# Optimization experiments

Measured on AMD Instinct MI355X. Metric: run time of the kernel, lower is better.

The kernel has to match this reference:

```python
import jax, jax.numpy as jnp
import numpy as np

MAXLEN = 30
VOCAB_SIZE = 20000
THOUGHT = 1200
WORD = 620
BATCH = 130  # decoder uses B-2 = 128 sequences


def setup_inputs() -> dict:
    key = jax.random.key(0)
    ks = jax.random.split(key, 8)
    s_ih = 1.0 / np.sqrt(WORD)
    return {
        "thoughts": jax.random.normal(ks[0], (BATCH, THOUGHT), dtype=jnp.float32),
        "embed_table": jax.random.normal(ks[1], (VOCAB_SIZE, WORD), dtype=jnp.float32),
        "W_ih": jax.random.uniform(ks[2], (4 * WORD, 2 * THOUGHT + WORD), jnp.float32, -s_ih, s_ih),
        "W_hh": jax.random.uniform(ks[3], (4 * WORD, WORD), jnp.float32, -s_ih, s_ih),
        "b_ih": jax.random.uniform(ks[4], (4 * WORD,), jnp.float32, -s_ih, s_ih),
        "b_hh": jax.random.uniform(ks[5], (4 * WORD,), jnp.float32, -s_ih, s_ih),
        "Ww": jax.random.uniform(ks[6], (VOCAB_SIZE, WORD), jnp.float32, -s_ih, s_ih),
        "bw": jax.random.uniform(ks[7], (VOCAB_SIZE,), jnp.float32, -s_ih, s_ih),
    }


def reference(thoughts, embed_table, W_ih, W_hh, b_ih, b_hh, Ww, bw):
    # context: concat(thoughts_prev, thoughts_next) -> [B-2, 2*THOUGHT]
    ctx = jnp.concatenate([thoughts[:-2], thoughts[2:]], axis=1)
    n = ctx.shape[0]
    h0 = jnp.zeros((n, WORD), dtype=thoughts.dtype)  # (h,c) reset to 0 each step

    def step(last_word, _):
        x = jnp.concatenate([ctx, last_word], axis=1)  # [n, 3020]
        # LSTM cell with zero initial state (original discards state each step)
        gates = x @ W_ih.T + b_ih + h0 @ W_hh.T + b_hh  # [n, 4*WORD]
        i, f, g, o = jnp.split(gates, 4, axis=1)
        c = jax.nn.sigmoid(i) * jnp.tanh(g)  # f-gate irrelevant, c_prev = 0
        h = jax.nn.sigmoid(o) * jnp.tanh(c)  # [n, WORD]
        logits = h @ Ww.T + bw               # [n, VOCAB]
        idx = jnp.argmax(logits, axis=1)
        new_last = embed_table[idx]          # greedy-decoded word embedding
        return new_last, h

    _, hs = jax.lax.scan(step, h0, None, length=MAXLEN)  # [MAXLEN, n, WORD]
    pred = jnp.einsum("tnw,vw->tnv", hs, Ww) + bw        # [MAXLEN, n, VOCAB]
    return jnp.transpose(pred, (1, 0, 2))                 # [n, MAXLEN, VOCAB]
```

## Files before the change

### kernel.cpp

```cpp
#include <hip/hip_runtime.h>
#include <math.h>

#define VOCAB 20000
#define WORD 620
#define NSEQ 128
#define TMAX 30
#define CTXK 2400
#define XK 3020
#define NBLK 256

typedef unsigned long long u64;
typedef __attribute__((ext_vector_type(8))) short short8;
typedef __attribute__((ext_vector_type(4))) float f32x4;

__device__ __forceinline__ unsigned ford(float f) {
    unsigned b = __float_as_uint(f);
    return (b & 0x80000000u) ? ~b : (b | 0x80000000u);
}
__device__ __forceinline__ unsigned short bf16rne(float x) {
    unsigned u = __float_as_uint(x);
    return (unsigned short)((u + 0x7fffu + ((u >> 16) & 1u)) >> 16);
}
__device__ __forceinline__ float bf16tof(unsigned short h) {
    return __uint_as_float(((unsigned)h) << 16);
}
__device__ __forceinline__ short8 ld8(const unsigned short* p) {
    return *(const short8*)p;
}
#define MFMA(a, b, c) __builtin_amdgcn_mfma_f32_16x16x32_bf16((a), (b), (c), 0, 0, 0)
#define VMW(N) asm volatile("s_waitcnt vmcnt(" #N ")" ::: "memory")
#define AL64(p) __hip_atomic_load((p), __ATOMIC_RELAXED, __HIP_MEMORY_SCOPE_AGENT)
#define AADD(p) __hip_atomic_fetch_add((p), 1u, __ATOMIC_RELAXED, __HIP_MEMORY_SCOPE_AGENT)
#define ALD(p) __hip_atomic_load((p), __ATOMIC_RELAXED, __HIP_MEMORY_SCOPE_AGENT)

__device__ __forceinline__ void gload_lds16(const void* g, void* l) {
    __builtin_amdgcn_global_load_lds((const __attribute__((address_space(1))) void*)g,
                                     (__attribute__((address_space(3))) void*)l,
                                     16, 0, 0);
}


__global__ __launch_bounds__(256) void kpack_w(const float* __restrict__ src,
                                               unsigned short* __restrict__ dst,
                                               int nvt, int nks, int col0,
                                               int ncols_valid, int src_ld,
                                               int nrows_valid, int rowmap) {
    int i = blockIdx.x * 256 + threadIdx.x;
    if (i >= nvt * nks * 512) return;
    int j = i & 7;
    int lane = (i >> 3) & 63;
    int t2 = i >> 9;
    int ks = t2 % nks;
    int vt = t2 / nks;
    int r = vt * 16 + (lane & 15);
    int k = ks * 32 + ((lane >> 4) << 3) + j;
    float x = 0.f;
    if (r < nrows_valid && k < ncols_valid) {
        int row = (rowmap == 1) ? ((r < 620) ? r : r + 620) : r;
        x = src[(size_t)row * src_ld + col0 + k];
    }
    unsigned short hi = bf16rne(x);
    unsigned short lo = bf16rne(x - bf16tof(hi));
    size_t ob = (size_t)t2 * 1024 + lane * 8 + j;
    dst[ob] = hi;
    dst[ob + 512] = lo;
}

__global__ __launch_bounds__(256) void kpack_ctx(const float* __restrict__ th,
                                                 unsigned short* __restrict__ dst) {
    int i = blockIdx.x * 256 + threadIdx.x;
    if (i >= 75 * 8 * 512) return;
    int j = i & 7;
    int lane = (i >> 3) & 63;
    int t2 = i >> 9;
    int mt = t2 & 7;
    int ks = t2 >> 3;
    int n = mt * 16 + (lane & 15);
    int k = ks * 32 + ((lane >> 4) << 3) + j;
    float x = (k < 1200) ? th[(size_t)n * 1200 + k]
                         : th[(size_t)(n + 2) * 1200 + (k - 1200)];
    unsigned short hi = bf16rne(x);
    unsigned short lo = bf16rne(x - bf16tof(hi));
    size_t ob = (size_t)t2 * 1024 + lane * 8 + j;
    dst[ob] = hi;
    dst[ob + 512] = lo;
}

__global__ __launch_bounds__(256) void kpack_embed(const float* __restrict__ embed,
                                                   unsigned short* __restrict__ ehi,
                                                   unsigned short* __restrict__ elo) {
    size_t i = (size_t)blockIdx.x * 256 + threadIdx.x;
    if (i >= (size_t)VOCAB * 640) return;
    int v = (int)(i / 640);
    int k = (int)(i % 640);
    float x = (k < WORD) ? embed[(size_t)v * WORD + k] : 0.f;
    unsigned short hi = bf16rne(x);
    ehi[i] = hi;
    elo[i] = bf16rne(x - bf16tof(hi));
}

__global__ __launch_bounds__(256) void ggemm(const unsigned short* __restrict__ Af,
                                             const unsigned short* __restrict__ Bf,
                                             const float* __restrict__ addRow,
                                             const float* __restrict__ addFull,
                                             float* __restrict__ outT,
                                             int nks, int nvt, int ldout) {
    int lane = threadIdx.x & 63, wv = threadIdx.x >> 6;
    int vtb = blockIdx.x * 8 + wv * 2;
    bool ok0 = vtb < nvt, ok1 = (vtb + 1) < nvt;
    f32x4 acc[8][2];
#pragma unroll
    for (int m = 0; m < 8; ++m) { acc[m][0] = (f32x4)0.f; acc[m][1] = (f32x4)0.f; }
    if (ok0) {
        const unsigned short* ap = Af + lane * 8;
        const unsigned short* bp0 = Bf + (size_t)vtb * nks * 1024 + lane * 8;
        const unsigned short* bp1 = bp0 + (size_t)nks * 1024;
        for (int ks = 0; ks < nks; ++ks) {
            short8 b0h = ld8(bp0), b0l = ld8(bp0 + 512);
            short8 ah[8], al[8];
#pragma unroll
            for (int m = 0; m < 8; ++m) {
                ah[m] = ld8(ap + m * 1024);
                al[m] = ld8(ap + m * 1024 + 512);
            }
#pragma unroll
            for (int m = 0; m < 8; ++m) {
                acc[m][0] = MFMA(ah[m], b0h, acc[m][0]);
                acc[m][0] = MFMA(ah[m], b0l, acc[m][0]);
                acc[m][0] = MFMA(al[m], b0h, acc[m][0]);
            }
            if (ok1) {
                short8 b1h = ld8(bp1), b1l = ld8(bp1 + 512);
#pragma unroll
                for (int m = 0; m < 8; ++m) {
                    acc[m][1] = MFMA(ah[m], b1h, acc[m][1]);
                    acc[m][1] = MFMA(ah[m], b1l, acc[m][1]);
                    acc[m][1] = MFMA(al[m], b1h, acc[m][1]);
                }
            }
            ap += 8192; bp0 += 1024; bp1 += 1024;
        }
    }
    int rbase = (lane >> 4) << 2;
    int cof = lane & 15;
#pragma unroll
    for (int v = 0; v < 2; ++v) {
        bool ok = v ? ok1 : ok0;
        if (!ok) continue;
        int col = (vtb + v) * 16 + cof;
        float ar = addRow ? addRow[col] : 0.f;
#pragma unroll
        for (int m = 0; m < 8; ++m) {
#pragma unroll
            for (int r = 0; r < 4; ++r) {
                int row = m * 16 + rbase + r;
                float x = acc[m][v][r] + ar;
                if (addFull) x += addFull[(size_t)row * ldout + col];
                outT[(size_t)row * ldout + col] = x;
            }
        }
    }
}

__global__ __launch_bounds__(256) void kinit3(unsigned* hf32, unsigned* slots32,
                                              float* bsum, unsigned* bar,
                                              const float* __restrict__ b_ih,
                                              const float* __restrict__ b_hh) {
    int i = blockIdx.x * 256 + threadIdx.x;
    if (i < 81920) hf32[i] = 0u;
    if (i < 7680) slots32[i] = 0u;
    if (i < 512) bar[i] = 0u;
    if (i < 1872) {
        float v = 0.f;
        if (i < 1860) {
            int row = (i < 620) ? i : i + 620;
            v = b_ih[row] + b_hh[row];
        }
        bsum[i] = v;
    }
}

__global__ __launch_bounds__(512, 2) void kmega(
    const unsigned short* __restrict__ embhi,
    const unsigned short* __restrict__ emblo,
    const unsigned short* __restrict__ Wgf3,
    const unsigned short* __restrict__ Wwf,
    const float* __restrict__ base,
    const float* __restrict__ bw,
    unsigned short* __restrict__ hf,
    u64* __restrict__ slots,
    float* __restrict__ out,
    unsigned* bar) {
    __shared__ char sBhi[102400];
    __shared__ char sA[3][16384];
    __shared__ u64 keybuf[128];
    const int tid = threadIdx.x;
    const int lane = tid & 63;
    const int wv = tid >> 6;
    const int bid = blockIdx.x;

    const int vt_lo = (int)(((long long)bid * 1250) / NBLK);
    const int vt_hi = (int)(((long long)(bid + 1) * 1250) / NBLK);
    const int nvt = vt_hi - vt_lo;
    const bool act = (wv < nvt);
    const int myvt = vt_lo + (act ? wv : 0);
    const bool gact = (bid < 39);

    const char* hfb = (const char*)hf;
    const char* wwb = (const char*)Wwf;
    const unsigned short* BbaseLo = Wwf + (size_t)myvt * 20480 + 512 + lane * 8;

    for (int i = wv; i < nvt * 20; i += 8) {
        const char* g = wwb + (size_t)(vt_lo + i / 20) * 40960 + (size_t)(i % 20) * 2048 + lane * 16;
        gload_lds16(g, sBhi + (size_t)i * 1024);
    }
    VMW(0);
    __syncthreads();

    u64 R[3][4];
    short8 Bl[4];

#define ISSUE(M)                                                               \
    do {                                                                       \
        const u64* ga_ = (const u64*)(hfb + (size_t)(M) * 16384 +              \
                                      wv * 2048 + lane * 16);                  \
        R[(M) % 3][0] = AL64(ga_ + 0);                                         \
        R[(M) % 3][1] = AL64(ga_ + 1);                                         \
        R[(M) % 3][2] = AL64(ga_ + 128);                                       \
        R[(M) % 3][3] = AL64(ga_ + 129);                                       \
        if (act) Bl[(M) % 4] = ld8(BbaseLo + (size_t)(M) * 1024);              \
    } while (0)

#define WRA(M)                                                                 \
    do {                                                                       \
        u64* da_ = (u64*)(sA[(M) % 3] + wv * 2048 + lane * 16);                \
        da_[0] = R[(M) % 3][0];                                                \
        da_[1] = R[(M) % 3][1];                                                \
        da_[128] = R[(M) % 3][2];                                              \
        da_[129] = R[(M) % 3][3];                                              \
    } while (0)

#define LSTEP(K)                                                               \
    do {                                                                       \
        if ((K) + 3 < 20) ISSUE((K) + 3);                                      \
        if ((K) <= 16) { if (act) { VMW(10); } else { VMW(8); } }              \
        else if ((K) == 17) { if (act) { VMW(5); } else { VMW(4); } }          \
        else { VMW(0); }                                                       \
        if ((K) + 1 < 20) WRA((K) + 1);                                        \
        asm volatile("s_waitcnt lgkmcnt(0)" ::: "memory");                     \
        __builtin_amdgcn_s_barrier();                                          \
        __builtin_amdgcn_sched_barrier(0);                                     \
        if (act) {                                                             \
            const unsigned short* ab_ = (const unsigned short*)sA[(K) % 3];    \
            short8 bh_ = ld8((const unsigned short*)(sBhi +                    \
                             (size_t)(wv * 20 + (K)) * 1024) + lane * 8);      \
            _Pragma("unroll")                                                  \
            for (int mt = 0; mt < 8; ++mt) {                                   \
                short8 ah_ = ld8(ab_ + mt * 1024 + lane * 8);                  \
                short8 al_ = ld8(ab_ + mt * 1024 + 512 + lane * 8);            \
                acc[mt] = MFMA(ah_, bh_, acc[mt]);                             \
                acc[mt] = MFMA(ah_, Bl[(K) % 4], acc[mt]);                     \
                acc[mt] = MFMA(al_, bh_, acc[mt]);                             \
            }                                                                  \
        }                                                                      \
    } while (0)

    for (int t = 0; t < TMAX; ++t) {
        if (gact) {
            if (t > 0) {
                if (tid == 0)
                    while (ALD(&bar[256]) < 16u * (unsigned)t)
                        __builtin_amdgcn_s_sleep(2);
                __syncthreads();
            }
            const int g_vt = bid;
            const int g_mt = wv;
            f32x4 aI = (f32x4)0.f, aG = (f32x4)0.f, aO = (f32x4)0.f;
            if (t > 0) {
                int n = g_mt * 16 + (lane & 15);
                u64 s = AL64(&slots[(size_t)(t - 1) * NSEQ + n]);
                unsigned idx = 0xFFFFFFFFu - (unsigned)(s & 0xFFFFFFFFull);
                const unsigned short* eh = embhi + (size_t)idx * 640 + ((lane >> 4) << 3);
                const unsigned short* el = emblo + (size_t)idx * 640 + ((lane >> 4) << 3);
                const unsigned short* bI = Wgf3 + (size_t)(0 * 39 + g_vt) * 20480 + lane * 8;
                const unsigned short* bG = Wgf3 + (size_t)(1 * 39 + g_vt) * 20480 + lane * 8;
                const unsigned short* bO = Wgf3 + (size_t)(2 * 39 + g_vt) * 20480 + lane * 8;
#pragma unroll 2
                for (int ks = 0; ks < 20; ++ks) {
                    short8 ah = ld8(eh + ks * 32);
                    short8 al = ld8(el + ks * 32);
                    short8 bIh = ld8(bI), bIl = ld8(bI + 512);
                    short8 bGh = ld8(bG), bGl = ld8(bG + 512);
                    short8 bOh = ld8(bO), bOl = ld8(bO + 512);
                    aI = MFMA(ah, bIh, aI); aI = MFMA(ah, bIl, aI); aI = MFMA(al, bIh, aI);
                    aG = MFMA(ah, bGh, aG); aG = MFMA(ah, bGl, aG); aG = MFMA(al, bGh, aG);
                    aO = MFMA(ah, bOh, aO); aO = MFMA(ah, bOl, aO); aO = MFMA(al, bOh, aO);
                    bI += 1024; bG += 1024; bO += 1024;
                }
            }
            int col = g_vt * 16 + (lane & 15);
            if (col < WORD) {
                int rbase = g_mt * 16 + ((lane >> 4) << 2);
#pragma unroll
                for (int r = 0; r < 4; ++r) {
                    int n = rbase + r;
                    float gi = aI[r] + base[(size_t)n * 1872 + col];
                    float gg = aG[r] + base[(size_t)n * 1872 + 620 + col];
                    float go = aO[r] + base[(size_t)n * 1872 + 1240 + col];
                    float si = 1.f / (1.f + expf(-gi));
                    float so = 1.f / (1.f + expf(-go));
                    float h = so * tanhf(si * tanhf(gg));
                    int pos = (((col >> 5) * 8 + (n >> 4)) * 1024) +
                              (((n & 15) + (((col & 31) >> 3) << 4)) * 8) + (col & 7);
                    unsigned short hi = bf16rne(h);
                    hf[pos] = hi;
                    hf[pos + 512] = bf16rne(h - bf16tof(hi));
                }
            }
            __syncthreads();
            if (tid == 0) {
                __threadfence();
                unsigned g = (unsigned)bid >> 3;
                unsigned sz = (g < 4) ? 8u : 7u;
                unsigned a = AADD(&bar[272 + g * 16]);
                if (a == (unsigned)(t + 1) * sz - 1u)
                    AADD(&bar[352]);
            }
        }

        if (tid < 128) keybuf[tid] = 0ull;
        if (tid == 0)
            while (ALD(&bar[352]) < 5u * (unsigned)(t + 1))
                __builtin_amdgcn_s_sleep(2);
        __syncthreads();

        f32x4 acc[8];
#pragma unroll
        for (int mt = 0; mt < 8; ++mt) acc[mt] = (f32x4)0.f;

        ISSUE(0);
        ISSUE(1);
        ISSUE(2);
        if (act) { VMW(10); } else { VMW(8); }
        WRA(0);

        LSTEP(0);  LSTEP(1);  LSTEP(2);  LSTEP(3);  LSTEP(4);
        LSTEP(5);  LSTEP(6);  LSTEP(7);  LSTEP(8);  LSTEP(9);
        LSTEP(10); LSTEP(11); LSTEP(12); LSTEP(13); LSTEP(14);
        LSTEP(15); LSTEP(16); LSTEP(17); LSTEP(18); LSTEP(19);

        int q = lane >> 4, cof = lane & 15;
        if (act) {
            int v = myvt * 16 + cof;
            float bwv = bw[v];
#pragma unroll
            for (int mt = 0; mt < 8; ++mt) {
#pragma unroll
                for (int r = 0; r < 4; ++r) {
                    int n = mt * 16 + q * 4 + r;
                    float x = acc[mt][r] + bwv;
                    u64 key = ((u64)ford(x) << 32) | (u64)(0xFFFFFFFFu - (unsigned)v);
#pragma unroll
                    for (int s2 = 1; s2 <= 8; s2 <<= 1) {
                        u64 o = __shfl_xor(key, s2, 64);
                        if (o > key) key = o;
                    }
                    if (cof == 0) atomicMax(&keybuf[n], key);
                }
            }
        }
        __syncthreads();
        if (tid < 128) {
            u64 k = keybuf[tid];
            if (k) atomicMax(&slots[(size_t)t * NSEQ + tid], k);
        }
        __syncthreads();
        if (tid == 0) {
            unsigned g = (unsigned)bid >> 4;
            unsigned a = AADD(&bar[g * 16]);
            if (a == (unsigned)(t + 1) * 16u - 1u)
                AADD(&bar[256]);
        }
        if (act) {
            int v = myvt * 16 + cof;
            float bwv = bw[v];
#pragma unroll
            for (int mt = 0; mt < 8; ++mt) {
#pragma unroll
                for (int r = 0; r < 4; ++r) {
                    int n = mt * 16 + q * 4 + r;
                    float x = acc[mt][r] + bwv;
                    __builtin_nontemporal_store(x, &out[((size_t)n * TMAX + t) * VOCAB + v]);
                }
            }
        }
    }
#undef LSTEP
#undef WRA
#undef ISSUE
}

__global__ __launch_bounds__(256) void kinit2(unsigned int* lastfrag32,
                                              unsigned int* hfrag32,
                                              unsigned int* slots32,
                                              float* bsum,
                                              const float* __restrict__ b_ih,
                                              const float* __restrict__ b_hh) {
    int i = blockIdx.x * 256 + threadIdx.x;
    if (i < 81920) { lastfrag32[i] = 0u; hfrag32[i] = 0u; }
    if (i < 7680) slots32[i] = 0u;
    if (i < 1872) {
        float v = 0.f;
        if (i < 1860) {
            int row = (i < 620) ? i : i + 620;
            v = b_ih[row] + b_hh[row];
        }
        bsum[i] = v;
    }
}

__global__ __launch_bounds__(256) void klogits2(const unsigned short* __restrict__ Hf,
                                                const unsigned short* __restrict__ Wf,
                                                const float* __restrict__ bw,
                                                float* __restrict__ out,
                                                u64* __restrict__ slots, int t) {
    __shared__ u64 keybuf[128];
    int tid = threadIdx.x;
    if (tid < 128) keybuf[tid] = 0ull;
    __syncthreads();
    int lane = tid & 63, wv = tid >> 6;
    int vtb = blockIdx.x * 8 + wv * 2;
    bool ok0 = vtb < 1250, ok1 = (vtb + 1) < 1250;
    f32x4 acc[8][2];
#pragma unroll
    for (int m = 0; m < 8; ++m) { acc[m][0] = (f32x4)0.f; acc[m][1] = (f32x4)0.f; }
    if (ok0) {
        const unsigned short* ap = Hf + lane * 8;
        const unsigned short* bp0 = Wf + (size_t)vtb * 20 * 1024 + lane * 8;
        const unsigned short* bp1 = bp0 + 20 * 1024;
#pragma unroll 2
        for (int ks = 0; ks < 20; ++ks) {
            short8 b0h = ld8(bp0), b0l = ld8(bp0 + 512);
            short8 ah[8], al[8];
#pragma unroll
            for (int m = 0; m < 8; ++m) {
                ah[m] = ld8(ap + m * 1024);
                al[m] = ld8(ap + m * 1024 + 512);
            }
#pragma unroll
            for (int m = 0; m < 8; ++m) {
                acc[m][0] = MFMA(ah[m], b0h, acc[m][0]);
                acc[m][0] = MFMA(ah[m], b0l, acc[m][0]);
                acc[m][0] = MFMA(al[m], b0h, acc[m][0]);
            }
            if (ok1) {
                short8 b1h = ld8(bp1), b1l = ld8(bp1 + 512);
#pragma unroll
                for (int m = 0; m < 8; ++m) {
                    acc[m][1] = MFMA(ah[m], b1h, acc[m][1]);
                    acc[m][1] = MFMA(ah[m], b1l, acc[m][1]);
                    acc[m][1] = MFMA(al[m], b1h, acc[m][1]);
                }
            }
            ap += 8192; bp0 += 1024; bp1 += 1024;
        }
    }
    int rbase = (lane >> 4) << 2;
    int cof = lane & 15;
    float bw0 = ok0 ? bw[vtb * 16 + cof] : 0.f;
    float bw1 = ok1 ? bw[(vtb + 1) * 16 + cof] : 0.f;
#pragma unroll
    for (int m = 0; m < 8; ++m) {
#pragma unroll
        for (int r = 0; r < 4; ++r) {
            int row = m * 16 + rbase + r;
            u64 km = 0ull;
            if (ok0) {
                int v = vtb * 16 + cof;
                float x = acc[m][0][r] + bw0;
                out[((size_t)row * TMAX + t) * VOCAB + v] = x;
                km = ((u64)ford(x) << 32) | (u64)(0xFFFFFFFFu - (unsigned)v);
            }
            if (ok1) {
                int v = (vtb + 1) * 16 + cof;
                float x = acc[m][1][r] + bw1;
                out[((size_t)row * TMAX + t) * VOCAB + v] = x;
                u64 k2 = ((u64)ford(x) << 32) | (u64)(0xFFFFFFFFu - (unsigned)v);
                if (k2 > km) km = k2;
            }
#pragma unroll
            for (int s2 = 1; s2 <= 8; s2 <<= 1) {
                u64 o = __shfl_xor(km, s2, 64);
                if (o > km) km = o;
            }
            if ((lane & 15) == 0 && km) atomicMax(&keybuf[row], km);
        }
    }
    __syncthreads();
    if (tid < 128) atomicMax(&slots[(size_t)t * NSEQ + tid], keybuf[tid]);
}

__global__ void kact(const float* __restrict__ gates,
                     unsigned short* __restrict__ hfrag) {
    int n = blockIdx.x;
    int k = threadIdx.x;
    if (k >= WORD) return;
    const float* g = gates + (size_t)n * 1872;
    float gi = g[k], gg = g[620 + k], go = g[1240 + k];
    float si = 1.f / (1.f + expf(-gi));
    float so = 1.f / (1.f + expf(-go));
    float h = so * tanhf(si * tanhf(gg));
    int ks = k >> 5, mt = n >> 4;
    int lane = (n & 15) + (((k & 31) >> 3) << 4);
    int j = k & 7;
    size_t ob = (size_t)(ks * 8 + mt) * 1024 + lane * 8 + j;
    unsigned short hi = bf16rne(h);
    hfrag[ob] = hi;
    hfrag[ob + 512] = bf16rne(h - bf16tof(hi));
}

__global__ void kgather2(const float* __restrict__ embed,
                         const u64* __restrict__ slots,
                         unsigned short* __restrict__ lastfrag, int t) {
    int n = blockIdx.x;
    int k = threadIdx.x;
    if (k >= WORD) return;
    u64 s = slots[(size_t)t * NSEQ + n];
    unsigned idx = 0xFFFFFFFFu - (unsigned)(s & 0xFFFFFFFFull);
    float x = embed[(size_t)idx * WORD + k];
    int ks = k >> 5, mt = n >> 4;
    int lane = (n & 15) + (((k & 31) >> 3) << 4);
    int j = k & 7;
    size_t ob = (size_t)(ks * 8 + mt) * 1024 + lane * 8 + j;
    unsigned short hi = bf16rne(x);
    lastfrag[ob] = hi;
    lastfrag[ob + 512] = bf16rne(x - bf16tof(hi));
}

extern "C" void kernel_launch(void* const* d_in, const int* in_sizes, int n_in,
                              void* d_out, int out_size, void* d_ws, size_t ws_size,
                              hipStream_t stream) {
    const float* thoughts = (const float*)d_in[0];
    const float* embed    = (const float*)d_in[1];
    const float* W_ih     = (const float*)d_in[2];
    const float* b_ih     = (const float*)d_in[4];
    const float* b_hh     = (const float*)d_in[5];
    const float* Ww       = (const float*)d_in[6];
    const float* bw       = (const float*)d_in[7];
    float* out = (float*)d_out;
    char* ws = (char*)d_ws;

    const size_t OFF_WWF  = 0;
    const size_t OFF_WBF  = 51200000;
    const size_t OFF_WGF3 = 69171200;
    const size_t OFF_CTXF = 73963520;
    const size_t OFF_EHI  = 75192320;
    const size_t OFF_ELO  = 100792320;
    const size_t OFF_HF   = 126392320;
    const size_t OFF_BASE = 126720000;
    const size_t OFF_BSUM = 127678464;
    const size_t OFF_SLOT = 127685952;
    const size_t OFF_BAR  = 127716672;
    const size_t NEED_MEGA = 127718720;

    if (ws_size >= NEED_MEGA) {
        unsigned short* Wwf  = (unsigned short*)(ws + OFF_WWF);
        unsigned short* Wbf  = (unsigned short*)(ws + OFF_WBF);
        unsigned short* Wgf3 = (unsigned short*)(ws + OFF_WGF3);
        unsigned short* ctxf = (unsigned short*)(ws + OFF_CTXF);
        unsigned short* ehi  = (unsigned short*)(ws + OFF_EHI);
        unsigned short* elo  = (unsigned short*)(ws + OFF_ELO);
        unsigned short* hf   = (unsigned short*)(ws + OFF_HF);
        float* base = (float*)(ws + OFF_BASE);
        float* bsum = (float*)(ws + OFF_BSUM);
        u64*   slots = (u64*)(ws + OFF_SLOT);
        unsigned* bar = (unsigned*)(ws + OFF_BAR);

        kinit3<<<320, 256, 0, stream>>>((unsigned*)hf, (unsigned*)slots, bsum, bar, b_ih, b_hh);
        kpack_w<<<50000, 256, 0, stream>>>(Ww, Wwf, 1250, 20, 0, 620, WORD, VOCAB, 0);
        kpack_w<<<17550, 256, 0, stream>>>(W_ih, Wbf, 117, 75, 0, 2400, XK, 1860, 1);
        kpack_w<<<1560, 256, 0, stream>>>(W_ih + (size_t)0 * XK,    Wgf3 + 0 * 798720, 39, 20, 2400, 620, XK, 620, 0);
        kpack_w<<<1560, 256, 0, stream>>>(W_ih + (size_t)1240 * XK, Wgf3 + 1 * 798720, 39, 20, 2400, 620, XK, 620, 0);
        kpack_w<<<1560, 256, 0, stream>>>(W_ih + (size_t)1860 * XK, Wgf3 + 2 * 798720, 39, 20, 2400, 620, XK, 620, 0);
        kpack_ctx<<<1200, 256, 0, stream>>>(thoughts, ctxf);
        kpack_embed<<<50000, 256, 0, stream>>>(embed, ehi, elo);
        ggemm<<<15, 256, 0, stream>>>(ctxf, Wbf, bsum, nullptr, base, 75, 117, 1872);

        kmega<<<NBLK, 512, 0, stream>>>(ehi, elo, Wgf3, Wwf, base, bw, hf, slots, out, bar);
    } else {
        const size_t F_WWF  = 0;
        const size_t F_WBF  = 51200000;
        const size_t F_WGF  = 69171200;
        const size_t F_CTXF = 73963520;
        const size_t F_HF   = 75192320;
        const size_t F_LF   = 75520000;
        const size_t F_BASE = 75847680;
        const size_t F_GATE = 76806144;
        const size_t F_BSUM = 77764608;
        const size_t F_SLOT = 77772096;

        unsigned short* Wwf  = (unsigned short*)(ws + F_WWF);
        unsigned short* Wbf  = (unsigned short*)(ws + F_WBF);
        unsigned short* Wgf  = (unsigned short*)(ws + F_WGF);
        unsigned short* ctxf = (unsigned short*)(ws + F_CTXF);
        unsigned short* hf   = (unsigned short*)(ws + F_HF);
        unsigned short* lf   = (unsigned short*)(ws + F_LF);
        float* base = (float*)(ws + F_BASE);
        float* gate = (float*)(ws + F_GATE);
        float* bsum = (float*)(ws + F_BSUM);
        u64*   slots = (u64*)(ws + F_SLOT);

        kinit2<<<320, 256, 0, stream>>>((unsigned int*)lf, (unsigned int*)hf,
                                        (unsigned int*)slots, bsum, b_ih, b_hh);
        kpack_w<<<50000, 256, 0, stream>>>(Ww, Wwf, 1250, 20, 0, 620, WORD, VOCAB, 0);
        kpack_w<<<17550, 256, 0, stream>>>(W_ih, Wbf, 117, 75, 0, 2400, XK, 1860, 1);
        kpack_w<<<4680, 256, 0, stream>>>(W_ih, Wgf, 117, 20, 2400, 620, XK, 1860, 1);
        kpack_ctx<<<1200, 256, 0, stream>>>(thoughts, ctxf);
        ggemm<<<15, 256, 0, stream>>>(ctxf, Wbf, bsum, nullptr, base, 75, 117, 1872);
        for (int t = 0; t < TMAX; ++t) {
            ggemm<<<15, 256, 0, stream>>>(lf, Wgf, nullptr, base, gate, 20, 117, 1872);
            kact<<<NSEQ, 640, 0, stream>>>(gate, hf);
            klogits2<<<157, 256, 0, stream>>>(hf, Wwf, bw, out, slots, t);
            if (t + 1 < TMAX)
                kgather2<<<NSEQ, 640, 0, stream>>>(embed, slots, lf, t);
        }
    }
}
```

Before: 1.572 ms.

## Rotate hidden-state buffers per timestep and load with plain 16-byte vector loads

Gives each timestep its own hidden-state buffer, reusing the no-longer-needed Wbf workspace region after ggemm. This removes the write-after-read hazard on a single shared buffer and allows ordinary 16-byte cached loads in place of atomic 64-bit loads. A 40th gate block writes zero padding columns, so the buffer needs no zero-initialisation and the barrier group sizes become uniform. The trade-off is a larger working set across timesteps, and the code relies on stale cache lines never being observed for a buffer that is written fresh at each step.

```diff
diff --git a/kernel.cpp b/kernel.cpp
--- a/kernel.cpp
+++ b/kernel.cpp
@@ -162,12 +162,11 @@
     }
 }
 
-__global__ __launch_bounds__(256) void kinit3(unsigned* hf32, unsigned* slots32,
+__global__ __launch_bounds__(256) void kinit3(unsigned* slots32,
                                               float* bsum, unsigned* bar,
                                               const float* __restrict__ b_ih,
                                               const float* __restrict__ b_hh) {
     int i = blockIdx.x * 256 + threadIdx.x;
-    if (i < 81920) hf32[i] = 0u;
     if (i < 7680) slots32[i] = 0u;
     if (i < 512) bar[i] = 0u;
     if (i < 1872) {
@@ -187,7 +186,7 @@
     const unsigned short* __restrict__ Wwf,
     const float* __restrict__ base,
     const float* __restrict__ bw,
-    unsigned short* __restrict__ hf,
+    unsigned short* __restrict__ hfrot,
     u64* __restrict__ slots,
     float* __restrict__ out,
     unsigned* bar) {
@@ -204,9 +203,8 @@
     const int nvt = vt_hi - vt_lo;
     const bool act = (wv < nvt);
     const int myvt = vt_lo + (act ? wv : 0);
-    const bool gact = (bid < 39);
-
-    const char* hfb = (const char*)hf;
+    const bool gact = (bid < 40);
+
     const char* wwb = (const char*)Wwf;
     const unsigned short* BbaseLo = Wwf + (size_t)myvt * 20480 + 512 + lane * 8;
 
@@ -217,34 +215,30 @@
     VMW(0);
     __syncthreads();
 
-    u64 R[3][4];
+    short8 RA[3][2];
     short8 Bl[4];
 
-#define ISSUE(M)                                                               \
+#define ISSUE(M, HFT)                                                          \
     do {                                                                       \
-        const u64* ga_ = (const u64*)(hfb + (size_t)(M) * 16384 +              \
-                                      wv * 2048 + lane * 16);                  \
-        R[(M) % 3][0] = AL64(ga_ + 0);                                         \
-        R[(M) % 3][1] = AL64(ga_ + 1);                                         \
-        R[(M) % 3][2] = AL64(ga_ + 128);                                       \
-        R[(M) % 3][3] = AL64(ga_ + 129);                                       \
+        const unsigned short* ga_ = (HFT) + (size_t)(M) * 8192 +               \
+                                    wv * 1024 + lane * 8;                      \
+        RA[(M) % 3][0] = ld8(ga_);                                             \
+        RA[(M) % 3][1] = ld8(ga_ + 512);                                       \
         if (act) Bl[(M) % 4] = ld8(BbaseLo + (size_t)(M) * 1024);              \
     } while (0)
 
 #define WRA(M)                                                                 \
     do {                                                                       \
-        u64* da_ = (u64*)(sA[(M) % 3] + wv * 2048 + lane * 16);                \
-        da_[0] = R[(M) % 3][0];                                                \
-        da_[1] = R[(M) % 3][1];                                                \
-        da_[128] = R[(M) % 3][2];                                              \
-        da_[129] = R[(M) % 3][3];                                              \
+        char* da_ = sA[(M) % 3] + wv * 2048 + lane * 16;                       \
+        *(short8*)da_ = RA[(M) % 3][0];                                        \
+        *(short8*)(da_ + 1024) = RA[(M) % 3][1];                               \
     } while (0)
 
-#define LSTEP(K)                                                               \
+#define LSTEP(K, HFT)                                                          \
     do {                                                                       \
-        if ((K) + 3 < 20) ISSUE((K) + 3);                                      \
-        if ((K) <= 16) { if (act) { VMW(10); } else { VMW(8); } }              \
-        else if ((K) == 17) { if (act) { VMW(5); } else { VMW(4); } }          \
+        if ((K) + 3 < 20) ISSUE((K) + 3, HFT);                                 \
+        if ((K) <= 16) { if (act) { VMW(6); } else { VMW(4); } }               \
+        else if ((K) == 17) { if (act) { VMW(3); } else { VMW(2); } }          \
         else { VMW(0); }                                                       \
         if ((K) + 1 < 20) WRA((K) + 1);                                        \
         asm volatile("s_waitcnt lgkmcnt(0)" ::: "memory");                     \
@@ -266,6 +260,7 @@
     } while (0)
 
     for (int t = 0; t < TMAX; ++t) {
+        unsigned short* hft = hfrot + (size_t)t * 163840;
         if (gact) {
             if (t > 0) {
                 if (tid == 0)
@@ -276,7 +271,7 @@
             const int g_vt = bid;
             const int g_mt = wv;
             f32x4 aI = (f32x4)0.f, aG = (f32x4)0.f, aO = (f32x4)0.f;
-            if (t > 0) {
+            if (t > 0 && g_vt < 39) {
                 int n = g_mt * 16 + (lane & 15);
                 u64 s = AL64(&slots[(size_t)(t - 1) * NSEQ + n]);
                 unsigned idx = 0xFFFFFFFFu - (unsigned)(s & 0xFFFFFFFFull);
@@ -299,31 +294,31 @@
                 }
             }
             int col = g_vt * 16 + (lane & 15);
-            if (col < WORD) {
-                int rbase = g_mt * 16 + ((lane >> 4) << 2);
-#pragma unroll
-                for (int r = 0; r < 4; ++r) {
-                    int n = rbase + r;
+            int rbase = g_mt * 16 + ((lane >> 4) << 2);
+#pragma unroll
+            for (int r = 0; r < 4; ++r) {
+                int n = rbase + r;
+                float h = 0.f;
+                if (col < WORD) {
                     float gi = aI[r] + base[(size_t)n * 1872 + col];
                     float gg = aG[r] + base[(size_t)n * 1872 + 620 + col];
                     float go = aO[r] + base[(size_t)n * 1872 + 1240 + col];
                     float si = 1.f / (1.f + expf(-gi));
                     float so = 1.f / (1.f + expf(-go));
-                    float h = so * tanhf(si * tanhf(gg));
-                    int pos = (((col >> 5) * 8 + (n >> 4)) * 1024) +
-                              (((n & 15) + (((col & 31) >> 3) << 4)) * 8) + (col & 7);
-                    unsigned short hi = bf16rne(h);
-                    hf[pos] = hi;
-                    hf[pos + 512] = bf16rne(h - bf16tof(hi));
+                    h = so * tanhf(si * tanhf(gg));
                 }
+                int pos = (((col >> 5) * 8 + (n >> 4)) * 1024) +
+                          (((n & 15) + (((col & 31) >> 3) << 4)) * 8) + (col & 7);
+                unsigned short hi = bf16rne(h);
+                hft[pos] = hi;
+                hft[pos + 512] = bf16rne(h - bf16tof(hi));
             }
             __syncthreads();
             if (tid == 0) {
                 __threadfence();
                 unsigned g = (unsigned)bid >> 3;
-                unsigned sz = (g < 4) ? 8u : 7u;
                 unsigned a = AADD(&bar[272 + g * 16]);
-                if (a == (unsigned)(t + 1) * sz - 1u)
+                if (a == (unsigned)(t + 1) * 8u - 1u)
                     AADD(&bar[352]);
             }
         }
@@ -338,16 +333,16 @@
 #pragma unroll
         for (int mt = 0; mt < 8; ++mt) acc[mt] = (f32x4)0.f;
 
-        ISSUE(0);
-        ISSUE(1);
-        ISSUE(2);
-        if (act) { VMW(10); } else { VMW(8); }
+        ISSUE(0, hft);
+        ISSUE(1, hft);
+        ISSUE(2, hft);
+        if (act) { VMW(6); } else { VMW(4); }
         WRA(0);
 
-        LSTEP(0);  LSTEP(1);  LSTEP(2);  LSTEP(3);  LSTEP(4);
-        LSTEP(5);  LSTEP(6);  LSTEP(7);  LSTEP(8);  LSTEP(9);
-        LSTEP(10); LSTEP(11); LSTEP(12); LSTEP(13); LSTEP(14);
-        LSTEP(15); LSTEP(16); LSTEP(17); LSTEP(18); LSTEP(19);
+        LSTEP(0, hft);  LSTEP(1, hft);  LSTEP(2, hft);  LSTEP(3, hft);  LSTEP(4, hft);
+        LSTEP(5, hft);  LSTEP(6, hft);  LSTEP(7, hft);  LSTEP(8, hft);  LSTEP(9, hft);
+        LSTEP(10, hft); LSTEP(11, hft); LSTEP(12, hft); LSTEP(13, hft); LSTEP(14, hft);
+        LSTEP(15, hft); LSTEP(16, hft); LSTEP(17, hft); LSTEP(18, hft); LSTEP(19, hft);
 
         int q = lane >> 4, cof = lane & 15;
         if (act) {
@@ -556,27 +551,26 @@
     const size_t OFF_CTXF = 73963520;
     const size_t OFF_EHI  = 75192320;
     const size_t OFF_ELO  = 100792320;
-    const size_t OFF_HF   = 126392320;
-    const size_t OFF_BASE = 126720000;
-    const size_t OFF_BSUM = 127678464;
-    const size_t OFF_SLOT = 127685952;
-    const size_t OFF_BAR  = 127716672;
-    const size_t NEED_MEGA = 127718720;
+    const size_t OFF_BASE = 126392320;
+    const size_t OFF_BSUM = 127350784;
+    const size_t OFF_SLOT = 127358272;
+    const size_t OFF_BAR  = 127388992;
+    const size_t NEED_MEGA = 127391040;
 
     if (ws_size >= NEED_MEGA) {
         unsigned short* Wwf  = (unsigned short*)(ws + OFF_WWF);
         unsigned short* Wbf  = (unsigned short*)(ws + OFF_WBF);
+        unsigned short* hfrot = (unsigned short*)(ws + OFF_WBF);
         unsigned short* Wgf3 = (unsigned short*)(ws + OFF_WGF3);
         unsigned short* ctxf = (unsigned short*)(ws + OFF_CTXF);
         unsigned short* ehi  = (unsigned short*)(ws + OFF_EHI);
         unsigned short* elo  = (unsigned short*)(ws + OFF_ELO);
-        unsigned short* hf   = (unsigned short*)(ws + OFF_HF);
         float* base = (float*)(ws + OFF_BASE);
         float* bsum = (float*)(ws + OFF_BSUM);
         u64*   slots = (u64*)(ws + OFF_SLOT);
         unsigned* bar = (unsigned*)(ws + OFF_BAR);
 
-        kinit3<<<320, 256, 0, stream>>>((unsigned*)hf, (unsigned*)slots, bsum, bar, b_ih, b_hh);
+        kinit3<<<320, 256, 0, stream>>>((unsigned*)slots, bsum, bar, b_ih, b_hh);
         kpack_w<<<50000, 256, 0, stream>>>(Ww, Wwf, 1250, 20, 0, 620, WORD, VOCAB, 0);
         kpack_w<<<17550, 256, 0, stream>>>(W_ih, Wbf, 117, 75, 0, 2400, XK, 1860, 1);
         kpack_w<<<1560, 256, 0, stream>>>(W_ih + (size_t)0 * XK,    Wgf3 + 0 * 798720, 39, 20, 2400, 620, XK, 620, 0);
@@ -586,7 +580,7 @@
         kpack_embed<<<50000, 256, 0, stream>>>(embed, ehi, elo);
         ggemm<<<15, 256, 0, stream>>>(ctxf, Wbf, bsum, nullptr, base, 75, 117, 1872);
 
-        kmega<<<NBLK, 512, 0, stream>>>(ehi, elo, Wgf3, Wwf, base, bw, hf, slots, out, bar);
+        kmega<<<NBLK, 512, 0, stream>>>(ehi, elo, Wgf3, Wwf, base, bw, hfrot, slots, out, bar);
     } else {
         const size_t F_WWF  = 0;
         const size_t F_WBF  = 51200000;
```

After: 1.546 ms. No clear change (-1.7%).
